# Performance work log

Hardware: AMD Instinct MI355X
Metric: run time of the kernel (lower is better)

## Reference

```python
import jax, jax.numpy as jnp
import numpy as np

H = 4   # num_heads
D = 32  # out_dim per head
NEG_SLOPE = 0.01  # torch F.leaky_relu default


def setup_inputs() -> dict:
    key = jax.random.key(0)
    ks = jax.random.split(key, 8)
    N, E, IN, ED = 50000, 600000, 128, 64
    node_feats = jax.random.normal(ks[0], (N, IN), dtype=jnp.float32)
    edge_feats = jax.random.normal(ks[1], (E, ED), dtype=jnp.float32)
    src = jax.random.randint(ks[2], (E,), 0, N, dtype=jnp.int32)
    dst = jax.random.randint(ks[3], (E,), 0, N, dtype=jnp.int32)
    # Xavier-ish scaled weights to keep softmax logits sane
    Wn = jax.random.normal(ks[4], (IN, H * D), dtype=jnp.float32) * (1.0 / np.sqrt(IN))
    We = jax.random.normal(ks[5], (ED, H * D), dtype=jnp.float32) * (1.0 / np.sqrt(ED))
    Wa = jax.random.normal(ks[6], (2 * D,), dtype=jnp.float32) * (1.0 / np.sqrt(2 * D))
    Wo = jax.random.normal(ks[7], (H * D, D), dtype=jnp.float32) * (1.0 / np.sqrt(H * D))
    return {"node_feats": node_feats, "edge_feats": edge_feats, "src": src,
            "dst": dst, "Wn": Wn, "We": We, "Wa": Wa, "Wo": Wo}


def reference(node_feats, edge_feats, src, dst, Wn, We, Wa, Wo):
    N = node_feats.shape[0]
    # projections -> [N,H,D] and [E,H,D]
    zn = (node_feats @ Wn).reshape(N, H, D)
    ze = (edge_feats @ We).reshape(-1, H, D)
    # edge attention logits: concat([z_src+z_e, z_dst+z_e]) @ Wa, leaky_relu
    zs = zn[src] + ze                              # [E,H,D]
    zd = zn[dst] + ze                              # [E,H,D]
    e = jnp.einsum('ehd,d->eh', zs, Wa[:D]) + jnp.einsum('ehd,d->eh', zd, Wa[D:])
    e = jax.nn.leaky_relu(e, NEG_SLOPE)            # [E,H]
    # segment softmax over incoming edges of each destination node
    emax = jax.ops.segment_max(e, dst, num_segments=N)       # [N,H]
    emax = jnp.where(jnp.isfinite(emax), emax, 0.0)          # empty segments
    ex = jnp.exp(e - emax[dst])                              # [E,H]
    denom = jax.ops.segment_sum(ex, dst, num_segments=N)     # [N,H]
    alpha = ex / denom[dst]                                  # [E,H]
    # weighted scatter-sum of edge messages
    agg = jax.ops.segment_sum(alpha[..., None] * ze, dst, num_segments=N)  # [N,H,D]
    # DGL update_all leaves zero-in-degree nodes with their projected feats
    deg = jax.ops.segment_sum(jnp.ones_like(dst, dtype=jnp.float32), dst, num_segments=N)
    z = jnp.where((deg > 0)[:, None, None], agg, zn)
    out = jax.nn.relu(z.reshape(N, H * D) @ Wo)   # activation=relu; dropout is identity in eval
    return out
```

## Files before the change

kernel.cpp:

```cpp
#include <hip/hip_runtime.h>
#include <math.h>

#define HH 4
#define DD 32
#define HD 128
#define INF 128
#define EDF 64
#define NEG 0.01f
#define NB 256
#define CHUNK 64
#define GS_AGG   2048
#define GS_NODES 1024

template <int CTRL>
__device__ __forceinline__ float dpp_add(float v) {
    int t = __builtin_amdgcn_update_dpp(0, __float_as_int(v), CTRL, 0xF, 0xF, true);
    return v + __int_as_float(t);
}
__device__ __forceinline__ float red16(float v) {
    v = dpp_add<0xB1>(v);
    v = dpp_add<0x4E>(v);
    v = dpp_add<0x141>(v);
    v = dpp_add<0x140>(v);
    return v;
}

__global__ void k_pre(const float* __restrict__ Wn, const float* __restrict__ We,
                      const float* __restrict__ Wa, const float* __restrict__ Wo,
                      float* __restrict__ WnA, float* __restrict__ WnB,
                      float* __restrict__ WeC, float* __restrict__ WeWo,
                      float* __restrict__ WnWo, int* __restrict__ deg, int N) {
    int b = blockIdx.x, tid = threadIdx.x;
    if (b >= 25) {
        int i = (b - 25) * 512 + tid;
        if (i < N) deg[i] = 0;
        return;
    }
    if (b < 16) {
        int t = b * 512 + tid;
        int j = t >> 5, o = t & 31;
        int h = j >> 6, k = j & 63;
        float a = 0.f;
        for (int d = 0; d < DD; ++d)
            a += We[k * HD + h * DD + d] * Wo[(h * DD + d) * DD + o];
        WeWo[t] = a;
    } else if (b < 24) {
        int u = (b - 16) * 512 + tid;
        int k = u >> 5, o = u & 31;
        float a = 0.f;
        for (int d = 0; d < HD; ++d)
            a += Wn[k * HD + d] * Wo[d * DD + o];
        WnWo[u] = a;
    } else {
        int k = tid >> 2, h = tid & 3;
        float a = 0.f, bb = 0.f;
        for (int d = 0; d < DD; ++d) {
            float w = Wn[k * HD + h * DD + d];
            a += w * Wa[d];
            bb += w * Wa[DD + d];
        }
        WnA[k * HH + h] = a;
        WnB[k * HH + h] = bb;
        if (k < EDF) {
            float c = 0.f;
            for (int d = 0; d < DD; ++d)
                c += We[k * HD + h * DD + d] * (Wa[d] + Wa[DD + d]);
            WeC[k * HH + h] = c;
        }
    }
}

__global__ void k_nodes(const float* __restrict__ X, const float* __restrict__ WnA,
                        const float* __restrict__ WnB, float* __restrict__ an,
                        float* __restrict__ bn, int N) {
    int wave = threadIdx.x >> 6, lane = threadIdx.x & 63;
    float4 wa0 = *(const float4*)(WnA + lane * 8);
    float4 wa1 = *(const float4*)(WnA + lane * 8 + 4);
    float4 wb0 = *(const float4*)(WnB + lane * 8);
    float4 wb1 = *(const float4*)(WnB + lane * 8 + 4);
    int stride = gridDim.x * 4;
    for (int n = blockIdx.x * 4 + wave; n < N; n += stride) {
        float2 x2 = *(const float2*)(X + (size_t)n * INF + lane * 2);
        float pa[HH], pb[HH];
        pa[0] = x2.x * wa0.x + x2.y * wa1.x;
        pa[1] = x2.x * wa0.y + x2.y * wa1.y;
        pa[2] = x2.x * wa0.z + x2.y * wa1.z;
        pa[3] = x2.x * wa0.w + x2.y * wa1.w;
        pb[0] = x2.x * wb0.x + x2.y * wb1.x;
        pb[1] = x2.x * wb0.y + x2.y * wb1.y;
        pb[2] = x2.x * wb0.z + x2.y * wb1.z;
        pb[3] = x2.x * wb0.w + x2.y * wb1.w;
#pragma unroll
        for (int off = 32; off; off >>= 1)
#pragma unroll
            for (int h = 0; h < HH; ++h) {
                pa[h] += __shfl_xor(pa[h], off);
                pb[h] += __shfl_xor(pb[h], off);
            }
        if (lane == 0)
#pragma unroll
            for (int h = 0; h < HH; ++h) {
                an[(size_t)n * HH + h] = pa[h];
                bn[(size_t)n * HH + h] = pb[h];
            }
    }
}

__global__ void k_hist(const int* __restrict__ dst, int* __restrict__ deg,
                       int* __restrict__ rank, int E) {
    int e = blockIdx.x * blockDim.x + threadIdx.x;
    if (e < E) rank[e] = atomicAdd(&deg[dst[e]], 1);
}
__global__ void k_scan1(const int* __restrict__ deg, int* __restrict__ partial,
                        int N, int chunk) {
    __shared__ int s[256];
    int tid = threadIdx.x;
    int i = blockIdx.x * chunk + tid;
    int v = (tid < chunk && i < N) ? deg[i] : 0;
    s[tid] = v; __syncthreads();
    for (int off = 128; off; off >>= 1) {
        if (tid < off) s[tid] += s[tid + off];
        __syncthreads();
    }
    if (tid == 0) partial[blockIdx.x] = s[0];
}
__global__ void k_scan2(const int* __restrict__ partial, int* __restrict__ pscan) {
    __shared__ int s[NB];
    int tid = threadIdx.x;
    int v = partial[tid];
    s[tid] = v; __syncthreads();
    for (int off = 1; off < NB; off <<= 1) {
        int t = (tid >= off) ? s[tid - off] : 0;
        __syncthreads();
        s[tid] += t;
        __syncthreads();
    }
    pscan[tid] = s[tid] - v;
}
__global__ void k_scan3(const int* __restrict__ deg, const int* __restrict__ pscan,
                        int* __restrict__ offs, int2* __restrict__ nd,
                        int N, int chunk) {
    __shared__ int s[256];
    int tid = threadIdx.x;
    int i = blockIdx.x * chunk + tid;
    int v = (tid < chunk && i < N) ? deg[i] : 0;
    s[tid] = v; __syncthreads();
    for (int off = 1; off < 256; off <<= 1) {
        int t = (tid >= off) ? s[tid - off] : 0;
        __syncthreads();
        s[tid] += t;
        __syncthreads();
    }
    if (tid < chunk && i < N) {
        int o = pscan[blockIdx.x] + s[tid] - v;
        offs[i] = o;
        nd[i] = make_int2(o, v);
    }
}
__global__ void k_perm(const int* __restrict__ src, const int* __restrict__ dst,
                       const int* __restrict__ offs, const int* __restrict__ rank,
                       const float* __restrict__ an, int* __restrict__ eids,
                       float4* __restrict__ anp, int E) {
    int e = blockIdx.x * blockDim.x + threadIdx.x;
    if (e < E) {
        int p = offs[dst[e]] + rank[e];
        eids[p] = e;
        anp[p] = *(const float4*)(an + (size_t)src[e] * HH);
    }
}

__global__ void k_agg(const float* __restrict__ EF, const float4* __restrict__ anp,
                      const float* __restrict__ bn, const float* __restrict__ WeC,
                      const int* __restrict__ eids, const int2* __restrict__ nd,
                      const float* __restrict__ WW, const float* __restrict__ X,
                      const float* __restrict__ WnWo, float* __restrict__ out, int N) {
    __shared__ float ww_s[256 * 32];
    __shared__ float pw[4][256];
    __shared__ int   ebuf[4][CHUNK];
    for (int i = threadIdx.x; i < 256 * 32; i += 256)
        ww_s[i] = WW[i];
    __syncthreads();

    int wave = threadIdx.x >> 6, lane = threadIdx.x & 63;
    int g = lane >> 4, q = lane & 15;
    int r8 = lane >> 3, c4 = (lane & 7) * 4;
    float4 c0 = *(const float4*)(WeC + (q * 4 + 0) * 4);
    float4 c1 = *(const float4*)(WeC + (q * 4 + 1) * 4);
    float4 c2 = *(const float4*)(WeC + (q * 4 + 2) * 4);
    float4 c3 = *(const float4*)(WeC + (q * 4 + 3) * 4);
    int stride = gridDim.x * 4;
    for (int n = blockIdx.x * 4 + wave; n < N; n += stride) {
        int2 sd = nd[n];
        int st = sd.x, dn = sd.y;
        if (dn == 0) {
            if (lane < 32) {
                float a = 0.f;
                for (int k = 0; k < INF; ++k)
                    a += X[(size_t)n * INF + k] * WnWo[k * DD + lane];
                out[(size_t)n * DD + lane] = fmaxf(a, 0.f);
            }
            continue;
        }
        float4 bn4 = *(const float4*)(bn + (size_t)n * HH);
        float4* abuf = (float4*)pw[wave];
        float4 gh0 = make_float4(0.f, 0.f, 0.f, 0.f);
        float4 gh1 = gh0, gh2 = gh0, gh3 = gh0;
        float den0 = 0.f, den1 = 0.f, den2 = 0.f, den3 = 0.f;
        for (int r0 = 0; r0 < dn; r0 += CHUNK) {
            int cnt = dn - r0; if (cnt > CHUNK) cnt = CHUNK;
            {
                int l2 = lane < cnt ? lane : cnt - 1;
                ebuf[wave][lane] = eids[st + r0 + l2];
                abuf[lane] = anp[(size_t)(st + r0 + l2)];
            }
            int nb4 = (cnt + 3) >> 2;
            int e = ebuf[wave][g];
            float4 xA = *(const float4*)(EF + (size_t)e * EDF + q * 4);
            e = ebuf[wave][(4 + g) & 63];
            float4 xB = *(const float4*)(EF + (size_t)e * EDF + q * 4);
            for (int i = 0; i < nb4; ++i) {
                e = ebuf[wave][((i + 2) * 4 + g) & 63];
                float4 xC = *(const float4*)(EF + (size_t)e * EDF + q * 4);
                float4 a4 = abuf[i * 4 + g];
                bool valid = (i * 4 + g) < cnt;
                float ae0 = red16(xA.x * c0.x + xA.y * c1.x + xA.z * c2.x + xA.w * c3.x);
                float ae1 = red16(xA.x * c0.y + xA.y * c1.y + xA.z * c2.y + xA.w * c3.y);
                float ae2 = red16(xA.x * c0.z + xA.y * c1.z + xA.z * c2.z + xA.w * c3.z);
                float ae3 = red16(xA.x * c0.w + xA.y * c1.w + xA.z * c2.w + xA.w * c3.w);
                float l0 = a4.x + bn4.x + ae0;
                float l1 = a4.y + bn4.y + ae1;
                float l2 = a4.z + bn4.z + ae2;
                float l3 = a4.w + bn4.w + ae3;
                float w0 = valid ? __expf(l0 > 0.f ? l0 : NEG * l0) : 0.f;
                float w1 = valid ? __expf(l1 > 0.f ? l1 : NEG * l1) : 0.f;
                float w2 = valid ? __expf(l2 > 0.f ? l2 : NEG * l2) : 0.f;
                float w3 = valid ? __expf(l3 > 0.f ? l3 : NEG * l3) : 0.f;
                gh0.x += w0 * xA.x; gh0.y += w0 * xA.y; gh0.z += w0 * xA.z; gh0.w += w0 * xA.w;
                gh1.x += w1 * xA.x; gh1.y += w1 * xA.y; gh1.z += w1 * xA.z; gh1.w += w1 * xA.w;
                gh2.x += w2 * xA.x; gh2.y += w2 * xA.y; gh2.z += w2 * xA.z; gh2.w += w2 * xA.w;
                gh3.x += w3 * xA.x; gh3.y += w3 * xA.y; gh3.z += w3 * xA.z; gh3.w += w3 * xA.w;
                den0 += w0; den1 += w1; den2 += w2; den3 += w3;
                xA = xB; xB = xC;
            }
        }
#pragma unroll
        for (int off = 16; off < 64; off <<= 1) {
            gh0.x += __shfl_xor(gh0.x, off); gh0.y += __shfl_xor(gh0.y, off);
            gh0.z += __shfl_xor(gh0.z, off); gh0.w += __shfl_xor(gh0.w, off);
            gh1.x += __shfl_xor(gh1.x, off); gh1.y += __shfl_xor(gh1.y, off);
            gh1.z += __shfl_xor(gh1.z, off); gh1.w += __shfl_xor(gh1.w, off);
            gh2.x += __shfl_xor(gh2.x, off); gh2.y += __shfl_xor(gh2.y, off);
            gh2.z += __shfl_xor(gh2.z, off); gh2.w += __shfl_xor(gh2.w, off);
            gh3.x += __shfl_xor(gh3.x, off); gh3.y += __shfl_xor(gh3.y, off);
            gh3.z += __shfl_xor(gh3.z, off); gh3.w += __shfl_xor(gh3.w, off);
            den0 += __shfl_xor(den0, off); den1 += __shfl_xor(den1, off);
            den2 += __shfl_xor(den2, off); den3 += __shfl_xor(den3, off);
        }
        float* G = pw[wave];
        float dsel = g == 0 ? den0 : g == 1 ? den1 : g == 2 ? den2 : den3;
        float4 gsel = g == 0 ? gh0 : g == 1 ? gh1 : g == 2 ? gh2 : gh3;
        float inv = 1.f / dsel;
        float4 gn;
        gn.x = gsel.x * inv; gn.y = gsel.y * inv;
        gn.z = gsel.z * inv; gn.w = gsel.w * inv;
        *(float4*)&G[lane * 4] = gn;
        float4 acc = make_float4(0.f, 0.f, 0.f, 0.f);
#pragma unroll 8
        for (int s = 0; s < 32; ++s) {
            int row = s * 8 + r8;
            float gv = G[row];
            float4 w4 = *(const float4*)&ww_s[row * 32 + c4];
            acc.x += gv * w4.x;
            acc.y += gv * w4.y;
            acc.z += gv * w4.z;
            acc.w += gv * w4.w;
        }
#pragma unroll
        for (int off = 8; off < 64; off <<= 1) {
            acc.x += __shfl_xor(acc.x, off);
            acc.y += __shfl_xor(acc.y, off);
            acc.z += __shfl_xor(acc.z, off);
            acc.w += __shfl_xor(acc.w, off);
        }
        if (lane < 8) {
            float4 o_;
            o_.x = fmaxf(acc.x, 0.f);
            o_.y = fmaxf(acc.y, 0.f);
            o_.z = fmaxf(acc.z, 0.f);
            o_.w = fmaxf(acc.w, 0.f);
            *(float4*)(out + (size_t)n * DD + lane * 4) = o_;
        }
    }
}

extern "C" void kernel_launch(void* const* d_in, const int* in_sizes, int n_in,
                              void* d_out, int out_size, void* d_ws, size_t ws_size,
                              hipStream_t stream) {
    const float* node_feats = (const float*)d_in[0];
    const float* edge_feats = (const float*)d_in[1];
    const int*   src        = (const int*)d_in[2];
    const int*   dst        = (const int*)d_in[3];
    const float* Wn         = (const float*)d_in[4];
    const float* We         = (const float*)d_in[5];
    const float* Wa         = (const float*)d_in[6];
    const float* Wo         = (const float*)d_in[7];
    float* out = (float*)d_out;
    int N = in_sizes[0] / INF;
    int E = in_sizes[2];

    char* p = (char*)d_ws;
    auto alloc = [&](size_t bytes) {
        char* r = p;
        p += (bytes + 255) & ~(size_t)255;
        return r;
    };
    float* WnA    = (float*)alloc((size_t)INF * HH * 4);
    float* WnB    = (float*)alloc((size_t)INF * HH * 4);
    float* WeC    = (float*)alloc((size_t)EDF * HH * 4);
    float* WeWo   = (float*)alloc((size_t)EDF * HH * DD * 4);
    float* WnWo   = (float*)alloc((size_t)INF * DD * 4);
    float* an     = (float*)alloc((size_t)N * HH * 4);
    float* bn     = (float*)alloc((size_t)N * HH * 4);
    float4* anp   = (float4*)alloc((size_t)E * 16);
    int* deg      = (int*)alloc((size_t)N * 4);
    int* offs     = (int*)alloc((size_t)N * 4);
    int2* nd      = (int2*)alloc((size_t)N * 8);
    int* rank     = (int*)alloc((size_t)E * 4);
    int* eids     = (int*)alloc((size_t)E * 4);
    int* partial  = (int*)alloc((size_t)NB * 4);
    int* pscan    = (int*)alloc((size_t)NB * 4);

    int chunk = (N + NB - 1) / NB;
    int preblk = 25 + (N + 511) / 512;

    hipLaunchKernelGGL(k_pre, dim3(preblk), dim3(512), 0, stream,
                       Wn, We, Wa, Wo, WnA, WnB, WeC, WeWo, WnWo, deg, N);
    hipLaunchKernelGGL(k_nodes, dim3(GS_NODES), dim3(256), 0, stream,
                       node_feats, WnA, WnB, an, bn, N);
    hipLaunchKernelGGL(k_hist, dim3((E + 255) / 256), dim3(256), 0, stream,
                       dst, deg, rank, E);
    hipLaunchKernelGGL(k_scan1, dim3(NB), dim3(256), 0, stream, deg, partial, N, chunk);
    hipLaunchKernelGGL(k_scan2, dim3(1), dim3(NB), 0, stream, partial, pscan);
    hipLaunchKernelGGL(k_scan3, dim3(NB), dim3(256), 0, stream, deg, pscan, offs, nd, N, chunk);
    hipLaunchKernelGGL(k_perm, dim3((E + 255) / 256), dim3(256), 0, stream,
                       src, dst, offs, rank, an, eids, anp, E);
    hipLaunchKernelGGL(k_agg, dim3(GS_AGG), dim3(256), 0, stream,
                       edge_feats, anp, bn, WeC, eids, nd, WeWo, node_feats, WnWo, out, N);
}
```

Before: 166.4 us.

## Split output projection out of aggregation into a separate batched GEMM kernel

The aggregation kernel now writes each node's normalized 256-wide aggregate to a workspace buffer instead of projecting it through the 32KB WeWo matrix it used to stage in shared memory per block. A new kernel loads tiles of 64 nodes and computes the output projection with weights reused across 8 nodes per thread, handling zero-in-degree nodes there. This cuts the shared-memory footprint and preload cost of the aggregation kernel, which should raise its occupancy, and amortizes weight loads. The cost is an extra launch plus a 51MB write and read round trip through global memory.

```diff
diff --git a/kernel.cpp b/kernel.cpp
--- a/kernel.cpp
+++ b/kernel.cpp
@@ -11,6 +11,7 @@
 #define CHUNK 64
 #define GS_AGG   2048
 #define GS_NODES 1024
+#define ONODES 64
 
 template <int CTRL>
 __device__ __forceinline__ float dpp_add(float v) {
@@ -172,35 +173,20 @@
 __global__ void k_agg(const float* __restrict__ EF, const float4* __restrict__ anp,
                       const float* __restrict__ bn, const float* __restrict__ WeC,
                       const int* __restrict__ eids, const int2* __restrict__ nd,
-                      const float* __restrict__ WW, const float* __restrict__ X,
-                      const float* __restrict__ WnWo, float* __restrict__ out, int N) {
-    __shared__ float ww_s[256 * 32];
+                      float* __restrict__ Ghat, int N) {
     __shared__ float pw[4][256];
     __shared__ int   ebuf[4][CHUNK];
-    for (int i = threadIdx.x; i < 256 * 32; i += 256)
-        ww_s[i] = WW[i];
-    __syncthreads();
-
     int wave = threadIdx.x >> 6, lane = threadIdx.x & 63;
     int g = lane >> 4, q = lane & 15;
-    int r8 = lane >> 3, c4 = (lane & 7) * 4;
     float4 c0 = *(const float4*)(WeC + (q * 4 + 0) * 4);
     float4 c1 = *(const float4*)(WeC + (q * 4 + 1) * 4);
-    float4 c2 = *(const float4*)(WeC + (q * 4 + 2) * 4);
+    float4 c2w = *(const float4*)(WeC + (q * 4 + 2) * 4);
     float4 c3 = *(const float4*)(WeC + (q * 4 + 3) * 4);
     int stride = gridDim.x * 4;
     for (int n = blockIdx.x * 4 + wave; n < N; n += stride) {
         int2 sd = nd[n];
         int st = sd.x, dn = sd.y;
-        if (dn == 0) {
-            if (lane < 32) {
-                float a = 0.f;
-                for (int k = 0; k < INF; ++k)
-                    a += X[(size_t)n * INF + k] * WnWo[k * DD + lane];
-                out[(size_t)n * DD + lane] = fmaxf(a, 0.f);
-            }
-            continue;
-        }
+        if (dn == 0) continue;
         float4 bn4 = *(const float4*)(bn + (size_t)n * HH);
         float4* abuf = (float4*)pw[wave];
         float4 gh0 = make_float4(0.f, 0.f, 0.f, 0.f);
@@ -223,10 +209,10 @@
                 float4 xC = *(const float4*)(EF + (size_t)e * EDF + q * 4);
                 float4 a4 = abuf[i * 4 + g];
                 bool valid = (i * 4 + g) < cnt;
-                float ae0 = red16(xA.x * c0.x + xA.y * c1.x + xA.z * c2.x + xA.w * c3.x);
-                float ae1 = red16(xA.x * c0.y + xA.y * c1.y + xA.z * c2.y + xA.w * c3.y);
-                float ae2 = red16(xA.x * c0.z + xA.y * c1.z + xA.z * c2.z + xA.w * c3.z);
-                float ae3 = red16(xA.x * c0.w + xA.y * c1.w + xA.z * c2.w + xA.w * c3.w);
+                float ae0 = red16(xA.x * c0.x + xA.y * c1.x + xA.z * c2w.x + xA.w * c3.x);
+                float ae1 = red16(xA.x * c0.y + xA.y * c1.y + xA.z * c2w.y + xA.w * c3.y);
+                float ae2 = red16(xA.x * c0.z + xA.y * c1.z + xA.z * c2w.z + xA.w * c3.z);
+                float ae3 = red16(xA.x * c0.w + xA.y * c1.w + xA.z * c2w.w + xA.w * c3.w);
                 float l0 = a4.x + bn4.x + ae0;
                 float l1 = a4.y + bn4.y + ae1;
                 float l2 = a4.z + bn4.z + ae2;
@@ -256,40 +242,53 @@
             den0 += __shfl_xor(den0, off); den1 += __shfl_xor(den1, off);
             den2 += __shfl_xor(den2, off); den3 += __shfl_xor(den3, off);
         }
-        float* G = pw[wave];
         float dsel = g == 0 ? den0 : g == 1 ? den1 : g == 2 ? den2 : den3;
         float4 gsel = g == 0 ? gh0 : g == 1 ? gh1 : g == 2 ? gh2 : gh3;
         float inv = 1.f / dsel;
         float4 gn;
         gn.x = gsel.x * inv; gn.y = gsel.y * inv;
         gn.z = gsel.z * inv; gn.w = gsel.w * inv;
-        *(float4*)&G[lane * 4] = gn;
-        float4 acc = make_float4(0.f, 0.f, 0.f, 0.f);
-#pragma unroll 8
-        for (int s = 0; s < 32; ++s) {
-            int row = s * 8 + r8;
-            float gv = G[row];
-            float4 w4 = *(const float4*)&ww_s[row * 32 + c4];
-            acc.x += gv * w4.x;
-            acc.y += gv * w4.y;
-            acc.z += gv * w4.z;
-            acc.w += gv * w4.w;
-        }
-#pragma unroll
-        for (int off = 8; off < 64; off <<= 1) {
-            acc.x += __shfl_xor(acc.x, off);
-            acc.y += __shfl_xor(acc.y, off);
-            acc.z += __shfl_xor(acc.z, off);
-            acc.w += __shfl_xor(acc.w, off);
-        }
-        if (lane < 8) {
-            float4 o_;
-            o_.x = fmaxf(acc.x, 0.f);
-            o_.y = fmaxf(acc.y, 0.f);
-            o_.z = fmaxf(acc.z, 0.f);
-            o_.w = fmaxf(acc.w, 0.f);
-            *(float4*)(out + (size_t)n * DD + lane * 4) = o_;
-        }
+        *(float4*)(Ghat + (size_t)n * 256 + lane * 4) = gn;
+    }
+}
+
+__global__ void k_out(const float* __restrict__ G, const float* __restrict__ WW,
+                      const float* __restrict__ X, const float* __restrict__ WnWo,
+                      const int2* __restrict__ nd, float* __restrict__ out, int N) {
+    __shared__ float4 gs[ONODES * 64];
+    int tid = threadIdx.x;
+    int nb0 = blockIdx.x * ONODES;
+    int nrem = N - nb0;
+    int nloc = nrem < ONODES ? nrem : ONODES;
+    const float4* Gbase = (const float4*)G + (size_t)nb0 * 64;
+    for (int i = tid; i < nloc * 64; i += 256)
+        gs[i] = Gbase[i];
+    __syncthreads();
+    int o = tid & 31, grp = tid >> 5;
+    int t0 = grp * 8;
+    float acc[8] = {0.f, 0.f, 0.f, 0.f, 0.f, 0.f, 0.f, 0.f};
+    for (int j4 = 0; j4 < 64; ++j4) {
+        float w0 = WW[(j4 * 4 + 0) * 32 + o];
+        float w1 = WW[(j4 * 4 + 1) * 32 + o];
+        float w2 = WW[(j4 * 4 + 2) * 32 + o];
+        float w3 = WW[(j4 * 4 + 3) * 32 + o];
+#pragma unroll
+        for (int t = 0; t < 8; ++t) {
+            float4 gv = gs[(t0 + t) * 64 + j4];
+            acc[t] += gv.x * w0 + gv.y * w1 + gv.z * w2 + gv.w * w3;
+        }
+    }
+#pragma unroll
+    for (int t = 0; t < 8; ++t) {
+        int n = nb0 + t0 + t;
+        if (n >= N) break;
+        float a = acc[t];
+        if (nd[n].y == 0) {
+            a = 0.f;
+            for (int k = 0; k < INF; ++k)
+                a += X[(size_t)n * INF + k] * WnWo[k * DD + o];
+        }
+        out[(size_t)n * DD + o] = fmaxf(a, 0.f);
     }
 }
 
@@ -322,6 +321,7 @@
     float* an     = (float*)alloc((size_t)N * HH * 4);
     float* bn     = (float*)alloc((size_t)N * HH * 4);
     float4* anp   = (float4*)alloc((size_t)E * 16);
+    float* Ghat   = (float*)alloc((size_t)N * 256 * 4);
     int* deg      = (int*)alloc((size_t)N * 4);
     int* offs     = (int*)alloc((size_t)N * 4);
     int2* nd      = (int2*)alloc((size_t)N * 8);
@@ -345,5 +345,7 @@
     hipLaunchKernelGGL(k_perm, dim3((E + 255) / 256), dim3(256), 0, stream,
                        src, dst, offs, rank, an, eids, anp, E);
     hipLaunchKernelGGL(k_agg, dim3(GS_AGG), dim3(256), 0, stream,
-                       edge_feats, anp, bn, WeC, eids, nd, WeWo, node_feats, WnWo, out, N);
-}
+                       edge_feats, anp, bn, WeC, eids, nd, Ghat, N);
+    hipLaunchKernelGGL(k_out, dim3((N + ONODES - 1) / ONODES), dim3(256), 0, stream,
+                       Ghat, WeWo, node_feats, WnWo, nd, out, N);
+}
```

Result: slower. 209.3 us (+25.8%).

## Pre-permute edge features into dst-sorted fp16 buffer for contiguous aggregation reads

Applied to the files above, without the earlier changes.

Adds a kernel that reads edge features in original order, converts them to fp16, and scatters them into destination-sorted order. The aggregation kernel then reads contiguous half-precision rows instead of gathering fp32 rows through an edge-id indirection. This trades a full extra pass over the edge features, plus a scattered write, for coalesced and halved reads in the main kernel. It also lowers the precision of the edge features used in the attention logits and the messages.

```diff
diff --git a/kernel.cpp b/kernel.cpp
--- a/kernel.cpp
+++ b/kernel.cpp
@@ -1,4 +1,5 @@
 #include <hip/hip_runtime.h>
+#include <hip/hip_fp16.h>
 #include <math.h>
 
 #define HH 4
@@ -11,6 +12,7 @@
 #define CHUNK 64
 #define GS_AGG   2048
 #define GS_NODES 1024
+#define GS_TC    1024
 
 template <int CTRL>
 __device__ __forceinline__ float dpp_add(float v) {
@@ -159,24 +161,41 @@
 }
 __global__ void k_perm(const int* __restrict__ src, const int* __restrict__ dst,
                        const int* __restrict__ offs, const int* __restrict__ rank,
-                       const float* __restrict__ an, int* __restrict__ eids,
+                       const float* __restrict__ an, int* __restrict__ pos_of,
                        float4* __restrict__ anp, int E) {
     int e = blockIdx.x * blockDim.x + threadIdx.x;
     if (e < E) {
         int p = offs[dst[e]] + rank[e];
-        eids[p] = e;
+        pos_of[e] = p;
         anp[p] = *(const float4*)(an + (size_t)src[e] * HH);
     }
 }
 
-__global__ void k_agg(const float* __restrict__ EF, const float4* __restrict__ anp,
+__global__ void k_tc(const float* __restrict__ EF, const int* __restrict__ pos_of,
+                     __half* __restrict__ EF16p, int E) {
+    int wave = threadIdx.x >> 6, lane = threadIdx.x & 63;
+    int g = lane >> 4, q = lane & 15;
+    int nq = (E + 3) >> 2;
+    int stride = gridDim.x * 4;
+    for (int i = blockIdx.x * 4 + wave; i < nq; i += stride) {
+        int e = i * 4 + g;
+        if (e >= E) continue;
+        float4 x4 = *(const float4*)(EF + (size_t)e * EDF + q * 4);
+        int p = pos_of[e];
+        __half2 h01 = __floats2half2_rn(x4.x, x4.y);
+        __half2 h23 = __floats2half2_rn(x4.z, x4.w);
+        uint2 u = make_uint2(*(unsigned*)&h01, *(unsigned*)&h23);
+        *(uint2*)(EF16p + (size_t)p * EDF + q * 4) = u;
+    }
+}
+
+__global__ void k_agg(const __half* __restrict__ EF16p, const float4* __restrict__ anp,
                       const float* __restrict__ bn, const float* __restrict__ WeC,
-                      const int* __restrict__ eids, const int2* __restrict__ nd,
-                      const float* __restrict__ WW, const float* __restrict__ X,
-                      const float* __restrict__ WnWo, float* __restrict__ out, int N) {
+                      const int2* __restrict__ nd, const float* __restrict__ WW,
+                      const float* __restrict__ X, const float* __restrict__ WnWo,
+                      float* __restrict__ out, int N) {
     __shared__ float ww_s[256 * 32];
     __shared__ float pw[4][256];
-    __shared__ int   ebuf[4][CHUNK];
     for (int i = threadIdx.x; i < 256 * 32; i += 256)
         ww_s[i] = WW[i];
     __syncthreads();
@@ -186,7 +205,7 @@
     int r8 = lane >> 3, c4 = (lane & 7) * 4;
     float4 c0 = *(const float4*)(WeC + (q * 4 + 0) * 4);
     float4 c1 = *(const float4*)(WeC + (q * 4 + 1) * 4);
-    float4 c2 = *(const float4*)(WeC + (q * 4 + 2) * 4);
+    float4 c2w = *(const float4*)(WeC + (q * 4 + 2) * 4);
     float4 c3 = *(const float4*)(WeC + (q * 4 + 3) * 4);
     int stride = gridDim.x * 4;
     for (int n = blockIdx.x * 4 + wave; n < N; n += stride) {
@@ -206,27 +225,30 @@
         float4 gh0 = make_float4(0.f, 0.f, 0.f, 0.f);
         float4 gh1 = gh0, gh2 = gh0, gh3 = gh0;
         float den0 = 0.f, den1 = 0.f, den2 = 0.f, den3 = 0.f;
+        int dn1 = dn - 1;
         for (int r0 = 0; r0 < dn; r0 += CHUNK) {
             int cnt = dn - r0; if (cnt > CHUNK) cnt = CHUNK;
             {
                 int l2 = lane < cnt ? lane : cnt - 1;
-                ebuf[wave][lane] = eids[st + r0 + l2];
                 abuf[lane] = anp[(size_t)(st + r0 + l2)];
             }
             int nb4 = (cnt + 3) >> 2;
-            int e = ebuf[wave][g];
-            float4 xA = *(const float4*)(EF + (size_t)e * EDF + q * 4);
-            e = ebuf[wave][(4 + g) & 63];
-            float4 xB = *(const float4*)(EF + (size_t)e * EDF + q * 4);
+            int rr = r0 + g; rr = rr < dn ? rr : dn1;
+            uint2 xAu = *(const uint2*)(EF16p + (size_t)(st + rr) * EDF + q * 4);
+            rr = r0 + 4 + g; rr = rr < dn ? rr : dn1;
+            uint2 xBu = *(const uint2*)(EF16p + (size_t)(st + rr) * EDF + q * 4);
             for (int i = 0; i < nb4; ++i) {
-                e = ebuf[wave][((i + 2) * 4 + g) & 63];
-                float4 xC = *(const float4*)(EF + (size_t)e * EDF + q * 4);
+                rr = r0 + (i + 2) * 4 + g; rr = rr < dn ? rr : dn1;
+                uint2 xCu = *(const uint2*)(EF16p + (size_t)(st + rr) * EDF + q * 4);
                 float4 a4 = abuf[i * 4 + g];
                 bool valid = (i * 4 + g) < cnt;
-                float ae0 = red16(xA.x * c0.x + xA.y * c1.x + xA.z * c2.x + xA.w * c3.x);
-                float ae1 = red16(xA.x * c0.y + xA.y * c1.y + xA.z * c2.y + xA.w * c3.y);
-                float ae2 = red16(xA.x * c0.z + xA.y * c1.z + xA.z * c2.z + xA.w * c3.z);
-                float ae3 = red16(xA.x * c0.w + xA.y * c1.w + xA.z * c2.w + xA.w * c3.w);
+                float2 f01 = __half22float2(*(const __half2*)&xAu.x);
+                float2 f23 = __half22float2(*(const __half2*)&xAu.y);
+                float xx = f01.x, xy = f01.y, xz = f23.x, xw = f23.y;
+                float ae0 = red16(xx * c0.x + xy * c1.x + xz * c2w.x + xw * c3.x);
+                float ae1 = red16(xx * c0.y + xy * c1.y + xz * c2w.y + xw * c3.y);
+                float ae2 = red16(xx * c0.z + xy * c1.z + xz * c2w.z + xw * c3.z);
+                float ae3 = red16(xx * c0.w + xy * c1.w + xz * c2w.w + xw * c3.w);
                 float l0 = a4.x + bn4.x + ae0;
                 float l1 = a4.y + bn4.y + ae1;
                 float l2 = a4.z + bn4.z + ae2;
@@ -235,12 +257,12 @@
                 float w1 = valid ? __expf(l1 > 0.f ? l1 : NEG * l1) : 0.f;
                 float w2 = valid ? __expf(l2 > 0.f ? l2 : NEG * l2) : 0.f;
                 float w3 = valid ? __expf(l3 > 0.f ? l3 : NEG * l3) : 0.f;
-                gh0.x += w0 * xA.x; gh0.y += w0 * xA.y; gh0.z += w0 * xA.z; gh0.w += w0 * xA.w;
-                gh1.x += w1 * xA.x; gh1.y += w1 * xA.y; gh1.z += w1 * xA.z; gh1.w += w1 * xA.w;
-                gh2.x += w2 * xA.x; gh2.y += w2 * xA.y; gh2.z += w2 * xA.z; gh2.w += w2 * xA.w;
-                gh3.x += w3 * xA.x; gh3.y += w3 * xA.y; gh3.z += w3 * xA.z; gh3.w += w3 * xA.w;
+                gh0.x += w0 * xx; gh0.y += w0 * xy; gh0.z += w0 * xz; gh0.w += w0 * xw;
+                gh1.x += w1 * xx; gh1.y += w1 * xy; gh1.z += w1 * xz; gh1.w += w1 * xw;
+                gh2.x += w2 * xx; gh2.y += w2 * xy; gh2.z += w2 * xz; gh2.w += w2 * xw;
+                gh3.x += w3 * xx; gh3.y += w3 * xy; gh3.z += w3 * xz; gh3.w += w3 * xw;
                 den0 += w0; den1 += w1; den2 += w2; den3 += w3;
-                xA = xB; xB = xC;
+                xAu = xBu; xBu = xCu;
             }
         }
 #pragma unroll
@@ -322,11 +344,12 @@
     float* an     = (float*)alloc((size_t)N * HH * 4);
     float* bn     = (float*)alloc((size_t)N * HH * 4);
     float4* anp   = (float4*)alloc((size_t)E * 16);
+    __half* EF16p = (__half*)alloc((size_t)E * EDF * 2);
     int* deg      = (int*)alloc((size_t)N * 4);
     int* offs     = (int*)alloc((size_t)N * 4);
     int2* nd      = (int2*)alloc((size_t)N * 8);
     int* rank     = (int*)alloc((size_t)E * 4);
-    int* eids     = (int*)alloc((size_t)E * 4);
+    int* pos_of   = (int*)alloc((size_t)E * 4);
     int* partial  = (int*)alloc((size_t)NB * 4);
     int* pscan    = (int*)alloc((size_t)NB * 4);
 
@@ -343,7 +366,9 @@
     hipLaunchKernelGGL(k_scan2, dim3(1), dim3(NB), 0, stream, partial, pscan);
     hipLaunchKernelGGL(k_scan3, dim3(NB), dim3(256), 0, stream, deg, pscan, offs, nd, N, chunk);
     hipLaunchKernelGGL(k_perm, dim3((E + 255) / 256), dim3(256), 0, stream,
-                       src, dst, offs, rank, an, eids, anp, E);
+                       src, dst, offs, rank, an, pos_of, anp, E);
+    hipLaunchKernelGGL(k_tc, dim3(GS_TC), dim3(256), 0, stream,
+                       edge_feats, pos_of, EF16p, E);
     hipLaunchKernelGGL(k_agg, dim3(GS_AGG), dim3(256), 0, stream,
-                       edge_feats, anp, bn, WeC, eids, nd, WeWo, node_feats, WnWo, out, N);
-}
+                       EF16p, anp, bn, WeC, nd, WeWo, node_feats, WnWo, out, N);
+}
```

Measured after the change: 204.2 us. 22.7% more time.
